# Performance work log

Hardware: AMD Instinct MI355X
Metric: run time of the kernel (lower is better)

## Reference

```python
import jax, jax.numpy as jnp
import numpy as np

EPS = 1e-5


def _edge_conv(x, W, gamma, beta, k):
    """x: (B,N,C); W: (O,2C). Returns (B,N,O)."""
    xx = jnp.sum(x * x, axis=2, keepdims=True)                 # (B,N,1)
    inner = jnp.einsum('bnc,bmc->bnm', x, x)                   # (B,N,N)
    dist = xx + jnp.swapaxes(xx, 1, 2) - 2.0 * inner           # squared dists
    idx = jax.lax.top_k(-dist, k)[1]                           # (B,N,k) smallest dists
    nbr = jax.vmap(lambda xb, ib: xb[ib])(x, idx)              # (B,N,k,C) gather
    xi = jnp.broadcast_to(x[:, :, None, :], nbr.shape)
    edge = jnp.concatenate([nbr - xi, xi], axis=-1)            # (B,N,k,2C)
    out = jnp.einsum('bnkc,oc->bnko', edge, W)                 # 1x1 conv (per-edge linear)
    mean = jnp.mean(out, axis=(0, 1, 2))                       # BatchNorm2d (training stats)
    var = jnp.var(out, axis=(0, 1, 2))
    out = (out - mean) / jnp.sqrt(var + EPS) * gamma + beta
    return jnp.max(jax.nn.relu(out), axis=2)                   # max over k -> (B,N,O)


def _layernorm(x, g, b):
    mu = jnp.mean(x, axis=-1, keepdims=True)
    v = jnp.var(x, axis=-1, keepdims=True)
    return (x - mu) / jnp.sqrt(v + EPS) * g + b


def setup_inputs() -> dict:
    key = jax.random.key(0)
    ks = jax.random.split(key, 12)
    B, N = 8, 2048
    C1, C2, C3, C4 = 64, 64, 128, 256
    feat = C1 + C2 + C3 + C4              # 512
    fc_in = 2 * feat                      # max+avg -> 1024
    H, L = 512, 256

    def w(k_, shape):
        fan_in = shape[-1]
        return jax.random.normal(k_, shape, dtype=jnp.float32) * (1.0 / np.sqrt(fan_in))

    return {
        'points': jax.random.normal(ks[0], (B, N, 3), dtype=jnp.float32),
        'W1': w(ks[1], (C1, 6)),  'g1': jnp.ones(C1), 'b1': jnp.zeros(C1),
        'W2': w(ks[2], (C2, 2 * C1)), 'g2': jnp.ones(C2), 'b2': jnp.zeros(C2),
        'W3': w(ks[3], (C3, 2 * C2)), 'g3': jnp.ones(C3), 'b3': jnp.zeros(C3),
        'W4': w(ks[4], (C4, 2 * C3)), 'g4': jnp.ones(C4), 'b4': jnp.zeros(C4),
        'fc1_w': w(ks[5], (H, fc_in)), 'fc1_b': jnp.zeros(H),
        'ln1_g': jnp.ones(H), 'ln1_b': jnp.zeros(H),
        'fc2_w': w(ks[6], (L, H)), 'fc2_b': jnp.zeros(L),
        'ln2_g': jnp.ones(L), 'ln2_b': jnp.zeros(L),
        'k': 20,
    }


def reference(points, W1, g1, b1, W2, g2, b2, W3, g3, b3, W4, g4, b4,
              fc1_w, fc1_b, ln1_g, ln1_b, fc2_w, fc2_b, ln2_g, ln2_b, k):
    x1 = _edge_conv(points, W1, g1, b1, k)   # (B,N,64)
    x2 = _edge_conv(x1, W2, g2, b2, k)       # (B,N,64)
    x3 = _edge_conv(x2, W3, g3, b3, k)       # (B,N,128)
    x4 = _edge_conv(x3, W4, g4, b4, k)       # (B,N,256)
    feat = jnp.concatenate([x1, x2, x3, x4], axis=-1)          # (B,N,512)
    g = jnp.concatenate([jnp.max(feat, axis=1), jnp.mean(feat, axis=1)], axis=-1)  # (B,1024)
    h = g @ fc1_w.T + fc1_b
    h = jax.nn.relu(_layernorm(h, ln1_g, ln1_b))
    z = h @ fc2_w.T + fc2_b
    return _layernorm(z, ln2_g, ln2_b)       # (B,256)
```

## Files before the change

### kernel.cpp

```cpp
#include <hip/hip_runtime.h>
#include <cstdint>
#include <cstddef>

static constexpr int Bb = 8;
static constexpr int Nn = 2048;
static constexpr int Kn = 20;
static constexpr float EPSV = 1e-5f;
static constexpr int JSENT = 1 << 30;


struct TransJobs {
    const float* in[6];
    float* out[6];
    int R[6];
    int Cc[6];
};

__global__ void transpose_all_kernel(TransJobs tj) {
    int m = blockIdx.y;
    int i = blockIdx.x * 256 + threadIdx.x;
    int total = tj.R[m] * tj.Cc[m];
    if (i < total) {
        int r = i / tj.Cc[m], c = i % tj.Cc[m];
        tj.out[m][(size_t)c * tj.R[m] + r] = tj.in[m][i];
    }
}


template<int C, int O>
__global__ void prep_kernel(const float* __restrict__ x, const float* __restrict__ wt,
                            float* __restrict__ z1, float* __restrict__ z2,
                            float* __restrict__ xx, float4* __restrict__ xp,
                            float* __restrict__ zp) {
    const int blk = blockIdx.x;
    const int tid = threadIdx.x;
    if (blk >= 1088) {
        zp[(blk - 1088) * 256 + tid] = 0.f;
        return;
    }
    if (blk >= 1024) {
        int i = (blk - 1024) * 256 + tid;
        const float* xr = x + (size_t)i * C;
        float s = 0.f;
        for (int c = 0; c < C; ++c) { float v = xr[c]; s += v * v; }
        xx[i] = s;
        if (C == 3) xp[i] = make_float4(xr[0], xr[1], xr[2], s);
        return;
    }
    constexpr int TP = 16;
    constexpr int G = 256 / O;
    constexpr int PP = TP / G;
    const int p0 = blk * TP;
    const int oo = tid % O;
    const int g = tid / O;
    __shared__ float xs[TP][(C < 4) ? 4 : C];
    for (int e = tid; e < TP * C; e += 256) {
        int p = e / C, c = e % C;
        xs[p][c] = x[(size_t)(p0 + p) * C + c];
    }
    __syncthreads();
    float a1[PP], a2[PP];
#pragma unroll
    for (int p = 0; p < PP; ++p) { a1[p] = 0.f; a2[p] = 0.f; }
    if constexpr (C % 4 == 0) {
        for (int c = 0; c < C; c += 4) {
            float w1[4], w2[4];
#pragma unroll
            for (int q = 0; q < 4; ++q) {
                w1[q] = wt[(size_t)(c + q) * O + oo];
                w2[q] = wt[(size_t)(C + c + q) * O + oo];
            }
#pragma unroll
            for (int p = 0; p < PP; ++p) {
                const float4 xv = *(const float4*)(&xs[g * PP + p][c]);
                a1[p] = fmaf(xv.w, w1[3], fmaf(xv.z, w1[2], fmaf(xv.y, w1[1], fmaf(xv.x, w1[0], a1[p]))));
                a2[p] = fmaf(xv.w, w2[3], fmaf(xv.z, w2[2], fmaf(xv.y, w2[1], fmaf(xv.x, w2[0], a2[p]))));
            }
        }
    } else {
        for (int c = 0; c < C; ++c) {
            float w1 = wt[(size_t)c * O + oo];
            float w2 = wt[(size_t)(C + c) * O + oo];
#pragma unroll
            for (int p = 0; p < PP; ++p) {
                float xv = xs[g * PP + p][c];
                a1[p] = fmaf(xv, w1, a1[p]);
                a2[p] = fmaf(xv, w2, a2[p]);
            }
        }
    }
#pragma unroll
    for (int p = 0; p < PP; ++p) {
        size_t row = (size_t)(p0 + g * PP + p) * O + oo;
        z1[row] = a1[p];
        z2[row] = a2[p];
    }
}


using half8 = __attribute__((ext_vector_type(8))) _Float16;
using f32x16 = __attribute__((ext_vector_type(16))) float;

template<int C>
__global__ __launch_bounds__(256, 2)
void gram_dist_kernel(const float* __restrict__ x, const float* __restrict__ xx,
                      float* __restrict__ dist, int b0, size_t dstride) {
    static_assert(C % 32 == 0, "CT=32 tiling");
    constexpr int CT = 32;
    const int b = b0 + blockIdx.z;
    int p = blockIdx.x, rblk = 0;
    while (p >= 16 - rblk) { p -= 16 - rblk; ++rblk; }
    const int cblk = rblk + p;
    const int i0 = rblk * 128, j0 = cblk * 128;
    const int tid = threadIdx.x;
    const int lane = tid & 63;
    const int wv = tid >> 6;
    const int wr = wv >> 1, wc = wv & 1;

    __shared__ __align__(16) unsigned char smem[32768];
    _Float16* const AH = (_Float16*)smem;
    _Float16* const AL = AH + 4096;
    _Float16* const BH = AH + 8192;
    _Float16* const BL = AH + 12288;
    float (*T)[132] = (float (*)[132])smem;

    const float* xb = x + (size_t)b * Nn * C;
    int sga[4];
    const float* sgs[4];
#pragma unroll
    for (int q = 0; q < 4; ++q) {
        int g = tid + 256 * q;
        int pnt = (g >> 2) & 127;
        int cb8 = g & 3;
        sga[q] = cb8 * 128 + (pnt & ~7) + ((pnt + 2 * cb8) & 7);
        sgs[q] = xb + (size_t)(((q < 2) ? i0 : j0) + pnt) * C + cb8 * 8;
    }

    int fa[2][2], fb[2][2];
#pragma unroll
    for (int ks = 0; ks < 2; ++ks)
#pragma unroll
        for (int mi = 0; mi < 2; ++mi) {
            int t8 = ks * 2 + (lane >> 5);
            int pa = wr * 64 + mi * 32 + (lane & 31);
            int pb = wc * 64 + mi * 32 + (lane & 31);
            fa[ks][mi] = t8 * 128 + (pa & ~7) + ((pa + 2 * t8) & 7);
            fb[ks][mi] = t8 * 128 + (pb & ~7) + ((pb + 2 * t8) & 7);
        }

    f32x16 ahh[2][2] = {};
    f32x16 axx[2][2] = {};

    for (int c0 = 0; c0 < C; c0 += CT) {
#pragma unroll
        for (int q = 0; q < 4; ++q) {
            const float4 f0 = *(const float4*)(sgs[q] + c0);
            const float4 f1 = *(const float4*)(sgs[q] + c0 + 4);
            float v[8] = {f0.x, f0.y, f0.z, f0.w, f1.x, f1.y, f1.z, f1.w};
            half8 hv, lv;
#pragma unroll
            for (int e = 0; e < 8; ++e) {
                _Float16 h = (_Float16)v[e];
                hv[e] = h;
                lv[e] = (_Float16)((v[e] - (float)h) * 4096.f);
            }
            _Float16* dh = (q < 2) ? AH : BH;
            _Float16* dl = (q < 2) ? AL : BL;
            *(half8*)(dh + sga[q] * 8) = hv;
            *(half8*)(dl + sga[q] * 8) = lv;
        }
        __syncthreads();
#pragma unroll
        for (int ks = 0; ks < 2; ++ks) {
            half8 ah[2], al[2], bh[2], bl[2];
#pragma unroll
            for (int mi = 0; mi < 2; ++mi) {
                ah[mi] = *(const half8*)(AH + fa[ks][mi] * 8);
                al[mi] = *(const half8*)(AL + fa[ks][mi] * 8);
                bh[mi] = *(const half8*)(BH + fb[ks][mi] * 8);
                bl[mi] = *(const half8*)(BL + fb[ks][mi] * 8);
            }
#pragma unroll
            for (int mi = 0; mi < 2; ++mi)
#pragma unroll
                for (int ni = 0; ni < 2; ++ni) {
                    ahh[mi][ni] = __builtin_amdgcn_mfma_f32_32x32x16_f16(ah[mi], bh[ni], ahh[mi][ni], 0, 0, 0);
                    axx[mi][ni] = __builtin_amdgcn_mfma_f32_32x32x16_f16(ah[mi], bl[ni], axx[mi][ni], 0, 0, 0);
                    axx[mi][ni] = __builtin_amdgcn_mfma_f32_32x32x16_f16(al[mi], bh[ni], axx[mi][ni], 0, 0, 0);
                }
        }
        __syncthreads();
    }

    const float* xxb = xx + (size_t)b * Nn;
    float xi[2][16];
#pragma unroll
    for (int mi = 0; mi < 2; ++mi)
#pragma unroll
        for (int g = 0; g < 4; ++g) {
            float4 t4 = *(const float4*)(xxb + i0 + wr * 64 + mi * 32 + 4 * (lane >> 5) + 8 * g);
            xi[mi][g * 4 + 0] = t4.x; xi[mi][g * 4 + 1] = t4.y;
            xi[mi][g * 4 + 2] = t4.z; xi[mi][g * 4 + 3] = t4.w;
        }
    float xj[2];
#pragma unroll
    for (int ni = 0; ni < 2; ++ni) xj[ni] = xxb[j0 + wc * 64 + ni * 32 + (lane & 31)];

    float* db = dist + (size_t)blockIdx.z * dstride;
#pragma unroll
    for (int mi = 0; mi < 2; ++mi)
#pragma unroll
        for (int ni = 0; ni < 2; ++ni) {
            const int col = j0 + wc * 64 + ni * 32 + (lane & 31);
#pragma unroll
            for (int r = 0; r < 16; ++r) {
                int row = i0 + wr * 64 + mi * 32 + (r & 3) + 8 * (r >> 2) + 4 * (lane >> 5);
                float inner = fmaf(axx[mi][ni][r], 2.44140625e-4f, ahh[mi][ni][r]);
                db[(size_t)row * Nn + col] = xi[mi][r] + xj[ni] - 2.f * inner;
            }
        }

    if (cblk > rblk) {
        const int rr = tid >> 3;
        const int c4 = (tid & 7) * 4;
#pragma unroll
        for (int m = 0; m < 4; ++m) {
            if (wc == (m >> 1)) {
#pragma unroll
                for (int mi = 0; mi < 2; ++mi)
#pragma unroll
                    for (int r = 0; r < 16; ++r) {
                        int ig = wr * 64 + mi * 32 + (r & 3) + 8 * (r >> 2) + 4 * (lane >> 5);
                        if ((m & 1) == 0) {
                            float inner = fmaf(axx[mi][0][r], 2.44140625e-4f, ahh[mi][0][r]);
                            T[lane & 31][ig] = xi[mi][r] + xj[0] - 2.f * inner;
                        } else {
                            float inner = fmaf(axx[mi][1][r], 2.44140625e-4f, ahh[mi][1][r]);
                            T[lane & 31][ig] = xi[mi][r] + xj[1] - 2.f * inner;
                        }
                    }
            }
            __syncthreads();
            float* orow = db + (size_t)(j0 + m * 32 + rr) * Nn + i0;
#pragma unroll
            for (int s = 0; s < 4; ++s)
                *(float4*)(orow + c4 + s * 32) = *(const float4*)&T[rr][c4 + s * 32];
            __syncthreads();
        }
    }
}


__device__ __forceinline__ bool lex_less(float v1, int j1, float v2, int j2) {
    return v1 < v2 || (v1 == v2 && j1 < j2);
}

template<int CTRL>
__device__ __forceinline__ float dpp_min_step(float v) {
    int x = __float_as_int(v);
    int y = __builtin_amdgcn_update_dpp(x, x, CTRL, 0xf, 0xf, false);
    return fminf(v, __int_as_float(y));
}

__device__ __forceinline__ float wave_min64(float v) {
    v = dpp_min_step<0x111>(v);
    v = dpp_min_step<0x112>(v);
    v = dpp_min_step<0x114>(v);
    v = dpp_min_step<0x118>(v);
    v = dpp_min_step<0x142>(v);
    v = dpp_min_step<0x143>(v);
    return __int_as_float(__builtin_amdgcn_readlane(__float_as_int(v), 63));
}

#define TOP4_INS(v, j)                                                            \
    {                                                                             \
        bool l3 = (v) < tv3;                                                      \
        if (l3) {                                                                 \
            bool l2 = (v) < tv2;                                                  \
            bool l1 = (v) < tv1;                                                  \
            bool l0 = (v) < tv0;                                                  \
            tv3 = l2 ? tv2 : (v);  tj3 = l2 ? tj2 : (j);                          \
            tv2 = l2 ? (l1 ? tv1 : (v)) : tv2;  tj2 = l2 ? (l1 ? tj1 : (j)) : tj2;\
            tv1 = l1 ? (l0 ? tv0 : (v)) : tv1;  tj1 = l1 ? (l0 ? tj0 : (j)) : tj1;\
            tv0 = l0 ? (v) : tv0;  tj0 = l0 ? (j) : tj0;                          \
        }                                                                         \
    }

__device__ __forceinline__ void top4_build(const float4* __restrict__ dr4, int lane,
                                           float lv, int lj,
                                           float& tv0, int& tj0, float& tv1, int& tj1,
                                           float& tv2, int& tj2, float& tv3, int& tj3) {
    tv0 = tv1 = tv2 = tv3 = 3e38f;
    tj0 = tj1 = tj2 = tj3 = JSENT;
#pragma unroll
    for (int q = 0; q < 8; ++q) {
        float4 f = dr4[q * 64 + lane];
        float vv[4] = {f.x, f.y, f.z, f.w};
#pragma unroll
        for (int c = 0; c < 4; ++c) {
            int j = (q * 64 + lane) * 4 + c;
            float v = vv[c];
            if (lex_less(lv, lj, v, j)) TOP4_INS(v, j)
        }
    }
}

#define TOPK_ROUNDS(REBUILD)                                                      \
    int myj = 0;                                                                  \
    for (int t = 0; t < Kn; ++t) {                                                \
        float bv = wave_min64(tv0);                                               \
        unsigned long long tied = __ballot(tv0 == bv);                            \
        int bj;                                                                   \
        if (__popcll(tied) == 1) {                                                \
            int winner = (int)(__ffsll(tied) - 1);                                \
            bj = __builtin_amdgcn_readlane(tj0, winner);                          \
        } else {                                                                  \
            float fv = (tv0 == bv) ? bv : 3e38f;                                  \
            int fj = (tv0 == bv) ? tj0 : JSENT;                                   \
            _Pragma("unroll")                                                     \
            for (int off = 1; off < 64; off <<= 1) {                              \
                float ov = __shfl_xor(fv, off);                                   \
                int oj = __shfl_xor(fj, off);                                     \
                if (lex_less(ov, oj, fv, fj)) { fv = ov; fj = oj; }               \
            }                                                                     \
            bj = fj;                                                              \
        }                                                                         \
        if (lane == t) myj = bj;                                                  \
        if (tv0 == bv && tj0 == bj) {                                             \
            tv0 = tv1; tj0 = tj1; tv1 = tv2; tj1 = tj2;                           \
            tv2 = tv3; tj2 = tj3; tv3 = 3e38f; tj3 = JSENT;                       \
            if (tj0 == JSENT) { REBUILD; }                                        \
        }                                                                         \
    }                                                                             \
    if (lane < Kn) orow[lane] = myj;

__global__ void topk_kernel(const float* __restrict__ dist, int* __restrict__ idxo,
                            int b0, size_t dstride, int rows_per_batch_only) {
    const int w = threadIdx.x >> 6;
    const int lane = threadIdx.x & 63;
    const int lin = blockIdx.x * 4 + w;
    int bz, i;
    if (rows_per_batch_only) { bz = 0; i = lin; }
    else { bz = lin >> 11; i = lin & (Nn - 1); }
    const int b = b0 + bz;
    const float4* dr4 = (const float4*)(dist + (size_t)bz * dstride + (size_t)i * Nn);

    float tv0, tv1, tv2, tv3;
    int tj0, tj1, tj2, tj3;
    top4_build(dr4, lane, -3e38f, -1, tv0, tj0, tv1, tj1, tv2, tj2, tv3, tj3);

    int* orow = idxo + ((size_t)b * Nn + i) * Kn;
    TOPK_ROUNDS(top4_build(dr4, lane, bv, bj, tv0, tj0, tv1, tj1, tv2, tj2, tv3, tj3))
}


__device__ __forceinline__ void top4_build_c3(const float4* __restrict__ xpb,
                                              float xi0, float xi1, float xi2, float xxi,
                                              int lane, float lv, int lj,
                                              float& tv0, int& tj0, float& tv1, int& tj1,
                                              float& tv2, int& tj2, float& tv3, int& tj3) {
    tv0 = tv1 = tv2 = tv3 = 3e38f;
    tj0 = tj1 = tj2 = tj3 = JSENT;
#pragma unroll
    for (int m = 0; m < 32; ++m) {
        int j = m * 64 + lane;
        float4 f = xpb[j];
        float acc = 0.f;
        acc = fmaf(xi0, f.x, acc);
        acc = fmaf(xi1, f.y, acc);
        acc = fmaf(xi2, f.z, acc);
        float v = xxi + f.w - 2.f * acc;
        if (lex_less(lv, lj, v, j)) TOP4_INS(v, j)
    }
}

__global__ void topk_c3_kernel(const float4* __restrict__ xp, int* __restrict__ idxo,
                               int b0, int rows_per_batch_only) {
    const int w = threadIdx.x >> 6;
    const int lane = threadIdx.x & 63;
    const int lin = blockIdx.x * 4 + w;
    int bz, i;
    if (rows_per_batch_only) { bz = 0; i = lin; }
    else { bz = lin >> 11; i = lin & (Nn - 1); }
    const int b = b0 + bz;
    const float4* xpb = xp + (size_t)b * Nn;
    const float4 fi = xpb[i];
    const float xi0 = fi.x, xi1 = fi.y, xi2 = fi.z, xxi = fi.w;

    float tv0, tv1, tv2, tv3;
    int tj0, tj1, tj2, tj3;
    top4_build_c3(xpb, xi0, xi1, xi2, xxi, lane, -3e38f, -1,
                  tv0, tj0, tv1, tj1, tv2, tj2, tv3, tj3);

    int* orow = idxo + ((size_t)b * Nn + i) * Kn;
    TOPK_ROUNDS(top4_build_c3(xpb, xi0, xi1, xi2, xxi, lane, bv, bj, \
                              tv0, tj0, tv1, tj1, tv2, tj2, tv3, tj3))
}


template<int O>
__global__ void edge_stats_kernel(const float* __restrict__ z1, const float* __restrict__ z2,
                                  const int* __restrict__ idx,
                                  float* __restrict__ vmax, float* __restrict__ vmin,
                                  float* __restrict__ ssum, float* __restrict__ ssq) {
    constexpr int TPP = O / 4;
    constexpr int PPB = 256 / TPP;
    const int p0 = blockIdx.x * PPB;
    const int tid = threadIdx.x;
    const int q = tid % TPP;
    const int p = tid / TPP;
    const int oo = q * 4;
    __shared__ int jl[PPB][Kn];
    for (int e = tid; e < PPB * Kn; e += 256)
        jl[e / Kn][e % Kn] = idx[(size_t)(p0 + e / Kn) * Kn + (e % Kn)];
    __syncthreads();
    const int bi = p0 + p;
    const int b = bi >> 11;
    const float4 zi1 = *(const float4*)(z1 + (size_t)bi * O + oo);
    const float4 zi2 = *(const float4*)(z2 + (size_t)bi * O + oo);
    float ax = zi2.x - zi1.x, ay = zi2.y - zi1.y, az = zi2.z - zi1.z, aw = zi2.w - zi1.w;
    float mxx = -3e38f, mxy = -3e38f, mxz = -3e38f, mxw = -3e38f;
    float mnx = 3e38f, mny = 3e38f, mnz = 3e38f, mnw = 3e38f;
    float sx = 0.f, sy = 0.f, sz = 0.f, sw = 0.f;
    float qx = 0.f, qy = 0.f, qz = 0.f, qw = 0.f;
    const float* zbase = z1 + ((size_t)b * Nn) * O + oo;
#pragma unroll
    for (int kk = 0; kk < Kn; ++kk) {
        int j = jl[p][kk];
        float4 v = *(const float4*)(zbase + (size_t)j * O);
        v.x += ax; v.y += ay; v.z += az; v.w += aw;
        mxx = fmaxf(mxx, v.x); mxy = fmaxf(mxy, v.y); mxz = fmaxf(mxz, v.z); mxw = fmaxf(mxw, v.w);
        mnx = fminf(mnx, v.x); mny = fminf(mny, v.y); mnz = fminf(mnz, v.z); mnw = fminf(mnw, v.w);
        sx += v.x; sy += v.y; sz += v.z; sw += v.w;
        qx = fmaf(v.x, v.x, qx); qy = fmaf(v.y, v.y, qy);
        qz = fmaf(v.z, v.z, qz); qw = fmaf(v.w, v.w, qw);
    }
    float4 mx4 = make_float4(mxx, mxy, mxz, mxw);
    float4 mn4 = make_float4(mnx, mny, mnz, mnw);
    *(float4*)(vmax + (size_t)bi * O + oo) = mx4;
    *(float4*)(vmin + (size_t)bi * O + oo) = mn4;
    __shared__ float4 ssm[256], sqq[256];
    ssm[tid] = make_float4(sx, sy, sz, sw);
    sqq[tid] = make_float4(qx, qy, qz, qw);
    __syncthreads();
    if (p == 0) {
#pragma unroll 4
        for (int pp = 1; pp < PPB; ++pp) {
            float4 s4 = ssm[pp * TPP + q];
            float4 q4 = sqq[pp * TPP + q];
            sx += s4.x; sy += s4.y; sz += s4.z; sw += s4.w;
            qx += q4.x; qy += q4.y; qz += q4.z; qw += q4.w;
        }
        int slot = blockIdx.x & 63;
        atomicAdd(&ssum[slot * O + oo + 0], sx);
        atomicAdd(&ssum[slot * O + oo + 1], sy);
        atomicAdd(&ssum[slot * O + oo + 2], sz);
        atomicAdd(&ssum[slot * O + oo + 3], sw);
        atomicAdd(&ssq[slot * O + oo + 0], qx);
        atomicAdd(&ssq[slot * O + oo + 1], qy);
        atomicAdd(&ssq[slot * O + oo + 2], qz);
        atomicAdd(&ssq[slot * O + oo + 3], qw);
    }
}


template<int O>
__global__ void apply_pool_kernel(const float* __restrict__ vmax, const float* __restrict__ vmin,
                                  const float* __restrict__ ssum, const float* __restrict__ ssq,
                                  const float* __restrict__ gamma, const float* __restrict__ beta,
                                  float* __restrict__ xout,
                                  float* __restrict__ pmax, float* __restrict__ psum, int obase) {
    constexpr int TPP = O / 4;
    constexpr int PP2 = 256 / TPP;
    constexpr int S = 128 / PP2;
    const int chunk = blockIdx.x;
    const int b = blockIdx.y;
    const int tid = threadIdx.x;
    const int q = tid % TPP;
    const int g = tid / TPP;
    const int oo = q * 4;
    __shared__ __align__(16) float lsc[O], lsh[O];
    for (int o = tid; o < O; o += 256) {
        float s = 0.f, qq = 0.f;
        for (int sl = 0; sl < 64; ++sl) { s += ssum[sl * O + o]; qq += ssq[sl * O + o]; }
        const float cnt = (float)Bb * (float)Nn * (float)Kn;
        float mu = s / cnt;
        float var = qq / cnt - mu * mu;
        float sc_ = gamma[o] / sqrtf(var + EPSV);
        lsc[o] = sc_;
        lsh[o] = beta[o] - mu * sc_;
    }
    __syncthreads();
    const float4 sc = *(const float4*)(lsc + oo);
    const float4 sh = *(const float4*)(lsh + oo);
    float pmx = -3e38f, pmy = -3e38f, pmz = -3e38f, pmw = -3e38f;
    float psx = 0.f, psy = 0.f, psz = 0.f, psw = 0.f;
    const int n0 = chunk * 128;
    for (int s = 0; s < S; ++s) {
        int n = n0 + g + s * PP2;
        size_t ix = ((size_t)b * Nn + n) * O + oo;
        float4 vx = *(const float4*)(vmax + ix);
        float4 vn = *(const float4*)(vmin + ix);
        float4 r;
        r.x = fmaxf(fmaf(sc.x >= 0.f ? vx.x : vn.x, sc.x, sh.x), 0.f);
        r.y = fmaxf(fmaf(sc.y >= 0.f ? vx.y : vn.y, sc.y, sh.y), 0.f);
        r.z = fmaxf(fmaf(sc.z >= 0.f ? vx.z : vn.z, sc.z, sh.z), 0.f);
        r.w = fmaxf(fmaf(sc.w >= 0.f ? vx.w : vn.w, sc.w, sh.w), 0.f);
        *(float4*)(xout + ix) = r;
        pmx = fmaxf(pmx, r.x); pmy = fmaxf(pmy, r.y);
        pmz = fmaxf(pmz, r.z); pmw = fmaxf(pmw, r.w);
        psx += r.x; psy += r.y; psz += r.z; psw += r.w;
    }
    __shared__ float4 sm[256], ss2[256];
    sm[tid] = make_float4(pmx, pmy, pmz, pmw);
    ss2[tid] = make_float4(psx, psy, psz, psw);
    __syncthreads();
    if (g == 0) {
#pragma unroll 4
        for (int gg = 1; gg < PP2; ++gg) {
            float4 m4 = sm[gg * TPP + q];
            float4 s4 = ss2[gg * TPP + q];
            pmx = fmaxf(pmx, m4.x); pmy = fmaxf(pmy, m4.y);
            pmz = fmaxf(pmz, m4.z); pmw = fmaxf(pmw, m4.w);
            psx += s4.x; psy += s4.y; psz += s4.z; psw += s4.w;
        }
        size_t pb = ((size_t)b * 16 + chunk) * 512 + obase + oo;
        *(float4*)(pmax + pb) = make_float4(pmx, pmy, pmz, pmw);
        *(float4*)(psum + pb) = make_float4(psx, psy, psz, psw);
    }
}


__global__ void head1_kernel(const float* __restrict__ pmax, const float* __restrict__ psum,
                             const float* __restrict__ fct1, float* __restrict__ hp1) {
    const int ks = blockIdx.x;
    const int b = blockIdx.y;
    const int tid = threadIdx.x;
    __shared__ float gxs[64];
    if (tid < 64) {
        int c = ks * 64 + tid;
        if (c < 512) {
            float mx = -3e38f;
            for (int ch = 0; ch < 16; ++ch)
                mx = fmaxf(mx, pmax[((size_t)b * 16 + ch) * 512 + c]);
            gxs[tid] = mx;
        } else {
            int e = c - 512;
            float s = 0.f;
            for (int ch = 0; ch < 16; ++ch)
                s += psum[((size_t)b * 16 + ch) * 512 + e];
            gxs[tid] = s * (1.f / (float)Nn);
        }
    }
    __syncthreads();
    float h0 = 0.f, h1 = 0.f;
    const float* w = fct1 + (size_t)(ks * 64) * 512;
    for (int c = 0; c < 64; ++c) {
        float gc = gxs[c];
        h0 = fmaf(gc, w[(size_t)c * 512 + tid], h0);
        h1 = fmaf(gc, w[(size_t)c * 512 + tid + 256], h1);
    }
    hp1[((size_t)b * 16 + ks) * 512 + tid] = h0;
    hp1[((size_t)b * 16 + ks) * 512 + tid + 256] = h1;
}

__global__ void head2_kernel(const float* __restrict__ hp1, const float* __restrict__ fc1b,
                             const float* __restrict__ ln1g, const float* __restrict__ ln1b,
                             float* __restrict__ hh) {
    const int b = blockIdx.x;
    const int tid = threadIdx.x;
    __shared__ float red[256];
    float h0 = fc1b[tid], h1 = fc1b[tid + 256];
    for (int ks = 0; ks < 16; ++ks) {
        h0 += hp1[((size_t)b * 16 + ks) * 512 + tid];
        h1 += hp1[((size_t)b * 16 + ks) * 512 + tid + 256];
    }
    red[tid] = h0 + h1;
    __syncthreads();
    for (int st = 128; st > 0; st >>= 1) { if (tid < st) red[tid] += red[tid + st]; __syncthreads(); }
    float mu = red[0] * (1.f / 512.f);
    __syncthreads();
    float d0 = h0 - mu, d1 = h1 - mu;
    red[tid] = d0 * d0 + d1 * d1;
    __syncthreads();
    for (int st = 128; st > 0; st >>= 1) { if (tid < st) red[tid] += red[tid + st]; __syncthreads(); }
    float rs = 1.f / sqrtf(red[0] * (1.f / 512.f) + EPSV);
    hh[(size_t)b * 512 + tid]       = fmaxf(d0 * rs * ln1g[tid] + ln1b[tid], 0.f);
    hh[(size_t)b * 512 + tid + 256] = fmaxf(d1 * rs * ln1g[tid + 256] + ln1b[tid + 256], 0.f);
}

__global__ void head3_kernel(const float* __restrict__ hh, const float* __restrict__ fct2,
                             float* __restrict__ hp2) {
    const int ks = blockIdx.x;
    const int b = blockIdx.y;
    const int tid = threadIdx.x;
    __shared__ float hs[128];
    if (tid < 128) hs[tid] = hh[(size_t)b * 512 + ks * 128 + tid];
    __syncthreads();
    float z = 0.f;
    const float* w = fct2 + (size_t)(ks * 128) * 256;
    for (int c = 0; c < 128; ++c)
        z = fmaf(hs[c], w[(size_t)c * 256 + tid], z);
    hp2[((size_t)b * 4 + ks) * 256 + tid] = z;
}

__global__ void head4_kernel(const float* __restrict__ hp2, const float* __restrict__ fc2b,
                             const float* __restrict__ ln2g, const float* __restrict__ ln2b,
                             float* __restrict__ out) {
    const int b = blockIdx.x;
    const int tid = threadIdx.x;
    __shared__ float red[256];
    float z = fc2b[tid];
    for (int ks = 0; ks < 4; ++ks) z += hp2[((size_t)b * 4 + ks) * 256 + tid];
    red[tid] = z;
    __syncthreads();
    for (int st = 128; st > 0; st >>= 1) { if (tid < st) red[tid] += red[tid + st]; __syncthreads(); }
    float mu2 = red[0] * (1.f / 256.f);
    __syncthreads();
    float dz = z - mu2;
    red[tid] = dz * dz;
    __syncthreads();
    for (int st = 128; st > 0; st >>= 1) { if (tid < st) red[tid] += red[tid + st]; __syncthreads(); }
    float rs2 = 1.f / sqrtf(red[0] * (1.f / 256.f) + EPSV);
    out[b * 256 + tid] = dz * rs2 * ln2g[tid] + ln2b[tid];
}


template<int C, int O>
static void run_layer(const float* x, const float* gamma, const float* beta,
                      float* xout, float* DIST, float* XX, float4* XP, int* IDX,
                      float* Z1, float* Z2,
                      float* VMX, float* VMN, float* SSUM, float* SSQ,
                      const float* WT, float* PMAX, float* PSUM, int obase, bool big,
                      hipStream_t stream) {
    prep_kernel<C, O><<<1216, 256, 0, stream>>>(x, WT, Z1, Z2, XX, XP, SSUM);
    if constexpr (C == 3) {
        if (big) {
            topk_c3_kernel<<<Bb * Nn / 4, 256, 0, stream>>>(XP, IDX, 0, 0);
        } else {
            for (int b = 0; b < Bb; ++b)
                topk_c3_kernel<<<Nn / 4, 256, 0, stream>>>(XP, IDX, b, 1);
        }
    } else {
        if (big) {
            gram_dist_kernel<C><<<dim3(136, 1, Bb), 256, 0, stream>>>(x, XX, DIST, 0, (size_t)Nn * Nn);
            topk_kernel<<<Bb * Nn / 4, 256, 0, stream>>>(DIST, IDX, 0, (size_t)Nn * Nn, 0);
        } else {
            for (int b = 0; b < Bb; ++b) {
                gram_dist_kernel<C><<<dim3(136, 1, 1), 256, 0, stream>>>(x, XX, DIST, b, 0);
                topk_kernel<<<Nn / 4, 256, 0, stream>>>(DIST, IDX, b, 0, 1);
            }
        }
    }
    edge_stats_kernel<O><<<Bb * Nn / (1024 / O), 256, 0, stream>>>(Z1, Z2, IDX, VMX, VMN, SSUM, SSQ);
    apply_pool_kernel<O><<<dim3(16, 8), 256, 0, stream>>>(VMX, VMN, SSUM, SSQ, gamma, beta,
                                                          xout, PMAX, PSUM, obase);
}

extern "C" void kernel_launch(void* const* d_in, const int* in_sizes, int n_in,
                              void* d_out, int out_size, void* d_ws, size_t ws_size,
                              hipStream_t stream) {
    const float* points = (const float*)d_in[0];
    const float* W1 = (const float*)d_in[1];
    const float* g1 = (const float*)d_in[2];
    const float* b1 = (const float*)d_in[3];
    const float* W2 = (const float*)d_in[4];
    const float* g2 = (const float*)d_in[5];
    const float* b2 = (const float*)d_in[6];
    const float* W3 = (const float*)d_in[7];
    const float* g3 = (const float*)d_in[8];
    const float* b3 = (const float*)d_in[9];
    const float* W4 = (const float*)d_in[10];
    const float* g4 = (const float*)d_in[11];
    const float* b4 = (const float*)d_in[12];
    const float* fc1_w = (const float*)d_in[13];
    const float* fc1_b = (const float*)d_in[14];
    const float* ln1g = (const float*)d_in[15];
    const float* ln1b = (const float*)d_in[16];
    const float* fc2_w = (const float*)d_in[17];
    const float* fc2_b = (const float*)d_in[18];
    const float* ln2g = (const float*)d_in[19];
    const float* ln2b = (const float*)d_in[20];

    float* ws = (float*)d_ws;
    const size_t BN = (size_t)Bb * Nn;
    const bool big = ws_size >= (size_t)59826688 * 4;

    size_t off = 0;
    auto take = [&](size_t n) { size_t o = off; off += n; return o; };
    float* DIST = ws + take(big ? (size_t)Bb * Nn * Nn : (size_t)Nn * Nn);
    float* XX   = ws + take(BN);
    float4* XP  = (float4*)(ws + take(BN * 4));
    int*   IDX  = (int*)(ws + take(BN * Kn));
    float* Z1   = ws + take(BN * 256);
    float* Z2   = ws + take(BN * 256);
    float* VMX  = ws + take(BN * 256);
    float* VMN  = ws + take(BN * 256);
    float* SSUM = ws + take(64 * 256);
    float* SSQ  = ws + take(64 * 256);
    float* WT1  = ws + take(384);
    float* WT2  = ws + take(8192);
    float* WT3  = ws + take(16384);
    float* WT4  = ws + take(65536);
    float* FCT1 = ws + take(524288);
    float* FCT2 = ws + take(131072);
    float* X1   = ws + take(BN * 64);
    float* X2   = ws + take(BN * 64);
    float* X3   = ws + take(BN * 128);
    float* X4   = ws + take(BN * 256);
    float* PMAX = ws + take((size_t)Bb * 16 * 512);
    float* PSUM = ws + take((size_t)Bb * 16 * 512);

    float* HP1 = DIST;
    float* HH  = DIST + 65536;
    float* HP2 = DIST + 65536 + 4096;

    TransJobs tj;
    tj.in[0] = W1;    tj.out[0] = WT1;  tj.R[0] = 64;  tj.Cc[0] = 6;
    tj.in[1] = W2;    tj.out[1] = WT2;  tj.R[1] = 64;  tj.Cc[1] = 128;
    tj.in[2] = W3;    tj.out[2] = WT3;  tj.R[2] = 128; tj.Cc[2] = 128;
    tj.in[3] = W4;    tj.out[3] = WT4;  tj.R[3] = 256; tj.Cc[3] = 256;
    tj.in[4] = fc1_w; tj.out[4] = FCT1; tj.R[4] = 512; tj.Cc[4] = 1024;
    tj.in[5] = fc2_w; tj.out[5] = FCT2; tj.R[5] = 256; tj.Cc[5] = 512;
    transpose_all_kernel<<<dim3(2048, 6), 256, 0, stream>>>(tj);

    run_layer<3, 64>(points, g1, b1, X1, DIST, XX, XP, IDX, Z1, Z2, VMX, VMN, SSUM, SSQ, WT1, PMAX, PSUM, 0, big, stream);
    run_layer<64, 64>(X1, g2, b2, X2, DIST, XX, XP, IDX, Z1, Z2, VMX, VMN, SSUM, SSQ, WT2, PMAX, PSUM, 64, big, stream);
    run_layer<64, 128>(X2, g3, b3, X3, DIST, XX, XP, IDX, Z1, Z2, VMX, VMN, SSUM, SSQ, WT3, PMAX, PSUM, 128, big, stream);
    run_layer<128, 256>(X3, g4, b4, X4, DIST, XX, XP, IDX, Z1, Z2, VMX, VMN, SSUM, SSQ, WT4, PMAX, PSUM, 256, big, stream);

    head1_kernel<<<dim3(16, 8), 256, 0, stream>>>(PMAX, PSUM, FCT1, HP1);
    head2_kernel<<<Bb, 256, 0, stream>>>(HP1, fc1_b, ln1g, ln1b, HH);
    head3_kernel<<<dim3(4, 8), 256, 0, stream>>>(HH, FCT2, HP2);
    head4_kernel<<<Bb, 256, 0, stream>>>(HP2, fc2_b, ln2g, ln2b, (float*)d_out);
}
```

Measured before the change: 579.1 us.

## Pack neighbor slot index into low mantissa bits of top-k keys

The top-k selection now stores the per-lane slot index in the low 5 mantissa bits of each distance, so each lane keeps only four float keys instead of value/index pairs. Ties disappear because keys are unique within a lane, and the winning lane comes from the ballot. This drops the shuffle-based tie-break path and the integer index registers, cutting register pressure and compare work. In exchange, distances lose 5 low mantissa bits, which can change neighbor order for near-equal distances, and across lanes the smallest lane wins a tie rather than the smallest index.

```diff
diff --git a/kernel.cpp b/kernel.cpp
--- a/kernel.cpp
+++ b/kernel.cpp
@@ -6,7 +6,6 @@
 static constexpr int Nn = 2048;
 static constexpr int Kn = 20;
 static constexpr float EPSV = 1e-5f;
-static constexpr int JSENT = 1 << 30;
 
 
 struct TransJobs {
@@ -251,10 +250,6 @@
 }
 
 
-__device__ __forceinline__ bool lex_less(float v1, int j1, float v2, int j2) {
-    return v1 < v2 || (v1 == v2 && j1 < j2);
-}
-
 template<int CTRL>
 __device__ __forceinline__ float dpp_min_step(float v) {
     int x = __float_as_int(v);
@@ -272,64 +267,52 @@
     return __int_as_float(__builtin_amdgcn_readlane(__float_as_int(v), 63));
 }
 
-#define TOP4_INS(v, j)                                                            \
+__device__ __forceinline__ float pack_key(float v, int m) {
+    return __int_as_float((__float_as_int(v) & ~31) | m);
+}
+
+#define TOP4_INS(v)                                                               \
     {                                                                             \
         bool l3 = (v) < tv3;                                                      \
         if (l3) {                                                                 \
             bool l2 = (v) < tv2;                                                  \
             bool l1 = (v) < tv1;                                                  \
             bool l0 = (v) < tv0;                                                  \
-            tv3 = l2 ? tv2 : (v);  tj3 = l2 ? tj2 : (j);                          \
-            tv2 = l2 ? (l1 ? tv1 : (v)) : tv2;  tj2 = l2 ? (l1 ? tj1 : (j)) : tj2;\
-            tv1 = l1 ? (l0 ? tv0 : (v)) : tv1;  tj1 = l1 ? (l0 ? tj0 : (j)) : tj1;\
-            tv0 = l0 ? (v) : tv0;  tj0 = l0 ? (j) : tj0;                          \
+            tv3 = l2 ? tv2 : (v);                                                 \
+            tv2 = l2 ? (l1 ? tv1 : (v)) : tv2;                                    \
+            tv1 = l1 ? (l0 ? tv0 : (v)) : tv1;                                    \
+            tv0 = l0 ? (v) : tv0;                                                 \
         }                                                                         \
     }
 
 __device__ __forceinline__ void top4_build(const float4* __restrict__ dr4, int lane,
-                                           float lv, int lj,
-                                           float& tv0, int& tj0, float& tv1, int& tj1,
-                                           float& tv2, int& tj2, float& tv3, int& tj3) {
+                                           float lvk,
+                                           float& tv0, float& tv1, float& tv2, float& tv3) {
     tv0 = tv1 = tv2 = tv3 = 3e38f;
-    tj0 = tj1 = tj2 = tj3 = JSENT;
 #pragma unroll
     for (int q = 0; q < 8; ++q) {
         float4 f = dr4[q * 64 + lane];
         float vv[4] = {f.x, f.y, f.z, f.w};
 #pragma unroll
         for (int c = 0; c < 4; ++c) {
-            int j = (q * 64 + lane) * 4 + c;
-            float v = vv[c];
-            if (lex_less(lv, lj, v, j)) TOP4_INS(v, j)
-        }
-    }
-}
-
-#define TOPK_ROUNDS(REBUILD)                                                      \
+            float vk = pack_key(vv[c], q * 4 + c);
+            if (vk > lvk) TOP4_INS(vk)
+        }
+    }
+}
+
+#define TOPK_ROUNDS(REBUILD, DECODE)                                              \
     int myj = 0;                                                                  \
     for (int t = 0; t < Kn; ++t) {                                                \
         float bv = wave_min64(tv0);                                               \
         unsigned long long tied = __ballot(tv0 == bv);                            \
-        int bj;                                                                   \
-        if (__popcll(tied) == 1) {                                                \
-            int winner = (int)(__ffsll(tied) - 1);                                \
-            bj = __builtin_amdgcn_readlane(tj0, winner);                          \
-        } else {                                                                  \
-            float fv = (tv0 == bv) ? bv : 3e38f;                                  \
-            int fj = (tv0 == bv) ? tj0 : JSENT;                                   \
-            _Pragma("unroll")                                                     \
-            for (int off = 1; off < 64; off <<= 1) {                              \
-                float ov = __shfl_xor(fv, off);                                   \
-                int oj = __shfl_xor(fj, off);                                     \
-                if (lex_less(ov, oj, fv, fj)) { fv = ov; fj = oj; }               \
-            }                                                                     \
-            bj = fj;                                                              \
-        }                                                                         \
+        int wl = (int)(__ffsll((long long)tied) - 1);                             \
+        int bm = __float_as_int(bv) & 31;                                         \
+        int bj = (DECODE);                                                        \
         if (lane == t) myj = bj;                                                  \
-        if (tv0 == bv && tj0 == bj) {                                             \
-            tv0 = tv1; tj0 = tj1; tv1 = tv2; tj1 = tj2;                           \
-            tv2 = tv3; tj2 = tj3; tv3 = 3e38f; tj3 = JSENT;                       \
-            if (tj0 == JSENT) { REBUILD; }                                        \
+        if (tv0 == bv && lane == wl) {                                            \
+            tv0 = tv1; tv1 = tv2; tv2 = tv3; tv3 = 3e38f;                         \
+            if (tv0 == 3e38f) { REBUILD; }                                        \
         }                                                                         \
     }                                                                             \
     if (lane < Kn) orow[lane] = myj;
@@ -346,31 +329,29 @@
     const float4* dr4 = (const float4*)(dist + (size_t)bz * dstride + (size_t)i * Nn);
 
     float tv0, tv1, tv2, tv3;
-    int tj0, tj1, tj2, tj3;
-    top4_build(dr4, lane, -3e38f, -1, tv0, tj0, tv1, tj1, tv2, tj2, tv3, tj3);
+    top4_build(dr4, lane, -3e38f, tv0, tv1, tv2, tv3);
 
     int* orow = idxo + ((size_t)b * Nn + i) * Kn;
-    TOPK_ROUNDS(top4_build(dr4, lane, bv, bj, tv0, tj0, tv1, tj1, tv2, tj2, tv3, tj3))
+    TOPK_ROUNDS(top4_build(dr4, lane, bv, tv0, tv1, tv2, tv3),
+                (bm >> 2) * 256 + wl * 4 + (bm & 3))
 }
 
 
 __device__ __forceinline__ void top4_build_c3(const float4* __restrict__ xpb,
                                               float xi0, float xi1, float xi2, float xxi,
-                                              int lane, float lv, int lj,
-                                              float& tv0, int& tj0, float& tv1, int& tj1,
-                                              float& tv2, int& tj2, float& tv3, int& tj3) {
+                                              int lane, float lvk,
+                                              float& tv0, float& tv1, float& tv2, float& tv3) {
     tv0 = tv1 = tv2 = tv3 = 3e38f;
-    tj0 = tj1 = tj2 = tj3 = JSENT;
 #pragma unroll
     for (int m = 0; m < 32; ++m) {
-        int j = m * 64 + lane;
-        float4 f = xpb[j];
+        float4 f = xpb[m * 64 + lane];
         float acc = 0.f;
         acc = fmaf(xi0, f.x, acc);
         acc = fmaf(xi1, f.y, acc);
         acc = fmaf(xi2, f.z, acc);
         float v = xxi + f.w - 2.f * acc;
-        if (lex_less(lv, lj, v, j)) TOP4_INS(v, j)
+        float vk = pack_key(v, m);
+        if (vk > lvk) TOP4_INS(vk)
     }
 }
 
@@ -388,13 +369,11 @@
     const float xi0 = fi.x, xi1 = fi.y, xi2 = fi.z, xxi = fi.w;
 
     float tv0, tv1, tv2, tv3;
-    int tj0, tj1, tj2, tj3;
-    top4_build_c3(xpb, xi0, xi1, xi2, xxi, lane, -3e38f, -1,
-                  tv0, tj0, tv1, tj1, tv2, tj2, tv3, tj3);
+    top4_build_c3(xpb, xi0, xi1, xi2, xxi, lane, -3e38f, tv0, tv1, tv2, tv3);
 
     int* orow = idxo + ((size_t)b * Nn + i) * Kn;
-    TOPK_ROUNDS(top4_build_c3(xpb, xi0, xi1, xi2, xxi, lane, bv, bj, \
-                              tv0, tj0, tv1, tj1, tv2, tj2, tv3, tj3))
+    TOPK_ROUNDS(top4_build_c3(xpb, xi0, xi1, xi2, xxi, lane, bv, tv0, tv1, tv2, tv3),
+                bm * 64 + wl)
 }
 
 
```

Measured after the change: 542.1 us. 6.4% less time.
